# Optimization experiments

Measured on AMD Instinct MI355X. Metric: run time of the kernel, lower is better.

## Reference

```python
import jax, jax.numpy as jnp
import numpy as np

B, D_IN = 4096, 1024
E, K = 16, 2
EMB = 256
H1, H2 = 2048, 1024  # hidden_units, hidden_units // 2
O = 512              # num_classes


def setup_inputs() -> dict:
    key = jax.random.key(0)
    ks = jax.random.split(key, 10)
    s = lambda *sh: 1.0 / np.sqrt(sh[-2] if len(sh) > 1 else 1.0)
    return {
        "x":   jax.random.normal(ks[0], (B, D_IN), jnp.float32),
        "Wr":  jax.random.normal(ks[1], (D_IN, EMB), jnp.float32) * (1.0 / np.sqrt(D_IN)),
        "br":  jnp.zeros((EMB,), jnp.float32),
        "emb": jax.random.normal(ks[2], (E, EMB), jnp.float32) * (1.0 / np.sqrt(EMB)),
        "W1":  jax.random.normal(ks[3], (E, D_IN, H1), jnp.float32) * (1.0 / np.sqrt(D_IN)),
        "b1":  jnp.zeros((E, H1), jnp.float32),
        "W2":  jax.random.normal(ks[4], (E, H1, H2), jnp.float32) * (1.0 / np.sqrt(H1)),
        "b2":  jnp.zeros((E, H2), jnp.float32),
        "W3":  jax.random.normal(ks[5], (E, H2, O), jnp.float32) * (1.0 / np.sqrt(H2)),
        "b3":  jnp.zeros((E, O), jnp.float32),
    }


def reference(x, Wr, br, emb, W1, b1, W2, b2, W3, b3):
    # Router query: [B, EMB]
    q = x @ Wr + br
    # Negative squared euclidean distance to expert embeddings -> scores [B, E]
    d2 = jnp.sum(jnp.square(q[:, None, :] - emb[None, :, :]), axis=-1)
    scores = -d2
    gating_probs = jax.nn.softmax(scores, axis=-1)  # [B, E]
    # Top-k selection + renormalized gates
    top_v, top_i = jax.lax.top_k(scores, K)          # [B, K]
    gates = jax.nn.softmax(top_v, axis=-1)           # [B, K]
    # All experts run on full batch (dense), batched over expert axis
    h1 = jax.nn.relu(jnp.einsum('bi,eih->beh', x, W1) + b1)   # [B, E, H1]
    h2 = jax.nn.relu(jnp.einsum('beh,ehm->bem', h1, W2) + b2)  # [B, E, H2]
    out = jnp.einsum('bem,emo->beo', h2, W3) + b3              # [B, E, O]
    # Gather top-k expert outputs per example and combine
    sel = jnp.take_along_axis(out, top_i[:, :, None], axis=1)  # [B, K, O]
    final = jnp.sum(sel * gates[:, :, None], axis=1)           # [B, O]
    return final, q, gating_probs
```

## Files before the change

kernel.cpp:

```cpp
#include <hip/hip_runtime.h>
#include <hip/hip_bf16.h>

using bf16 = __hip_bfloat16;
typedef __attribute__((ext_vector_type(8))) short bf16x8;
typedef __attribute__((ext_vector_type(8))) unsigned short u16x8;
typedef __attribute__((ext_vector_type(4))) float f32x4;

constexpr int BATCH = 4096;
constexpr int D_IN  = 1024;
constexpr int NEXP  = 16;
constexpr int EMB   = 256;
constexpr int H1    = 2048;
constexpr int H2    = 1024;
constexpr int OUTD  = 512;
constexpr int SLOTS = BATCH * 2;
constexpr int SLOTS_PAD = SLOTS + 128;
constexpr int MAX_TILES = SLOTS / 128 + NEXP;

constexpr size_t WS_XB     = 0;
constexpr size_t WS_H1     = WS_XB     + (size_t)BATCH * D_IN * 2;
constexpr size_t WS_H2     = WS_H1     + (size_t)SLOTS_PAD * H1 * 2;
constexpr size_t WS_OSL    = WS_H2     + (size_t)SLOTS_PAD * H2 * 2;
constexpr size_t WS_TOPI   = WS_OSL    + (size_t)SLOTS_PAD * OUTD * 4;
constexpr size_t WS_GATES  = WS_TOPI   + (size_t)SLOTS * 4;
constexpr size_t WS_SLOTOF = WS_GATES  + (size_t)SLOTS * 4;
constexpr size_t WS_TOKL   = WS_SLOTOF + (size_t)SLOTS * 4;
constexpr size_t WS_CNT    = WS_TOKL   + (size_t)SLOTS_PAD * 4;
constexpr size_t WS_TMAP   = WS_CNT    + 64 * 4;
constexpr size_t WS_WT     = ((WS_TMAP + (size_t)MAX_TILES * 8) + 255) & ~(size_t)255;

__device__ __forceinline__ unsigned short f2bf(float f) {
    bf16 h = __float2bfloat16(f);
    return __builtin_bit_cast(unsigned short, h);
}

__device__ __forceinline__ void gload16(const unsigned short* g, unsigned short* l) {
    __builtin_amdgcn_global_load_lds(
        (const __attribute__((address_space(1))) unsigned int*)g,
        (__attribute__((address_space(3))) unsigned int*)l, 16, 0, 0);
}

__global__ __launch_bounds__(256) void k_cvt_x(const float* __restrict__ x,
                                               unsigned short* __restrict__ xb) {
    int i = blockIdx.x * 256 + threadIdx.x;
    float4 v = reinterpret_cast<const float4*>(x)[i];
    ushort4 o;
    o.x = f2bf(v.x); o.y = f2bf(v.y); o.z = f2bf(v.z); o.w = f2bf(v.w);
    reinterpret_cast<ushort4*>(xb)[i] = o;
}

__global__ __launch_bounds__(256) void k_wtrans(const float* __restrict__ W,
                                                unsigned short* __restrict__ Wt,
                                                int KD, int ND) {
    __shared__ float Tf[64][65];
    int e = blockIdx.z;
    int n0 = blockIdx.x * 64, k0 = blockIdx.y * 64;
    const float* Wb = W + ((size_t)e * KD + k0) * ND + n0;
    int t  = threadIdx.x;
    int kr = t >> 4, c4 = (t & 15) * 4;
#pragma unroll
    for (int i = 0; i < 4; i++) {
        float4 v = *reinterpret_cast<const float4*>(Wb + (size_t)(kr + i * 16) * ND + c4);
        Tf[kr + i * 16][c4 + 0] = v.x; Tf[kr + i * 16][c4 + 1] = v.y;
        Tf[kr + i * 16][c4 + 2] = v.z; Tf[kr + i * 16][c4 + 3] = v.w;
    }
    __syncthreads();
    unsigned short* Wtb = Wt + ((size_t)e * ND + n0) * KD + k0;
#pragma unroll
    for (int i = 0; i < 2; i++) {
        int idx = t + i * 256;
        int n = idx >> 3, ck = (idx & 7) * 8;
        u16x8 o;
#pragma unroll
        for (int j = 0; j < 8; j++) o[j] = f2bf(Tf[ck + j][n]);
        *reinterpret_cast<u16x8*>(Wtb + (size_t)n * KD + ck) = o;
    }
}

__global__ __launch_bounds__(256) void k_router_gemm(const float* __restrict__ x,
                                                     const float* __restrict__ Wr,
                                                     const float* __restrict__ br,
                                                     float* __restrict__ qout) {
    __shared__ float As[64][17];
    __shared__ float Bs[16][68];
    int mb = blockIdx.x * 64, nb = blockIdx.y * 64;
    int t  = threadIdx.x;
    int tx = t & 15, ty = t >> 4;
    float acc[4][4] = {};
    int arow = t >> 2, ak = (t & 3) * 4;
    int bkr = t >> 4, bnc = (t & 15) * 4;
    for (int kt = 0; kt < D_IN; kt += 16) {
        float4 av = *reinterpret_cast<const float4*>(&x[(size_t)(mb + arow) * D_IN + kt + ak]);
        float4 bv = *reinterpret_cast<const float4*>(&Wr[(size_t)(kt + bkr) * EMB + nb + bnc]);
        As[arow][ak + 0] = av.x; As[arow][ak + 1] = av.y;
        As[arow][ak + 2] = av.z; As[arow][ak + 3] = av.w;
        Bs[bkr][bnc + 0] = bv.x; Bs[bkr][bnc + 1] = bv.y;
        Bs[bkr][bnc + 2] = bv.z; Bs[bkr][bnc + 3] = bv.w;
        __syncthreads();
#pragma unroll
        for (int k = 0; k < 16; k++) {
            float a[4], bb[4];
#pragma unroll
            for (int i = 0; i < 4; i++) a[i] = As[ty * 4 + i][k];
#pragma unroll
            for (int j = 0; j < 4; j++) bb[j] = Bs[k][tx * 4 + j];
#pragma unroll
            for (int i = 0; i < 4; i++)
#pragma unroll
                for (int j = 0; j < 4; j++) acc[i][j] = fmaf(a[i], bb[j], acc[i][j]);
        }
        __syncthreads();
    }
#pragma unroll
    for (int i = 0; i < 4; i++) {
        int row = mb + ty * 4 + i;
        float4 o;
        o.x = acc[i][0] + br[nb + tx * 4 + 0];
        o.y = acc[i][1] + br[nb + tx * 4 + 1];
        o.z = acc[i][2] + br[nb + tx * 4 + 2];
        o.w = acc[i][3] + br[nb + tx * 4 + 3];
        *reinterpret_cast<float4*>(&qout[(size_t)row * EMB + nb + tx * 4]) = o;
    }
}

__global__ __launch_bounds__(256) void k_router_topk(const float* __restrict__ q,
                                                     const float* __restrict__ emb,
                                                     float* __restrict__ gp,
                                                     int* __restrict__ topi,
                                                     float* __restrict__ gates) {
    int b    = blockIdx.x * 4 + (threadIdx.x >> 6);
    int lane = threadIdx.x & 63;
    int e    = lane & 15;
    int seg  = (lane >> 4) * 64;
    const float* qr = q + (size_t)b * EMB + seg;
    const float* er = emb + (size_t)e * EMB + seg;
    float d2 = 0.f;
#pragma unroll 8
    for (int i = 0; i < 64; i++) { float d = qr[i] - er[i]; d2 = fmaf(d, d, d2); }
    d2 += __shfl_xor(d2, 16);
    d2 += __shfl_xor(d2, 32);
    float s = -d2;
    float m = s;
#pragma unroll
    for (int o = 1; o < 16; o <<= 1) m = fmaxf(m, __shfl_xor(m, o));
    float ex  = __expf(s - m);
    float sum = ex;
#pragma unroll
    for (int o = 1; o < 16; o <<= 1) sum += __shfl_xor(sum, o);
    if (lane < 16) gp[(size_t)b * NEXP + lane] = ex / sum;
    float v1 = s; int i1 = e;
#pragma unroll
    for (int o = 1; o < 16; o <<= 1) {
        float ov = __shfl_xor(v1, o); int oi = __shfl_xor(i1, o);
        if (ov > v1 || (ov == v1 && oi < i1)) { v1 = ov; i1 = oi; }
    }
    float s2 = (e == i1) ? -1e30f : s;
    float v2 = s2; int i2 = e;
#pragma unroll
    for (int o = 1; o < 16; o <<= 1) {
        float ov = __shfl_xor(v2, o); int oi = __shfl_xor(i2, o);
        if (ov > v2 || (ov == v2 && oi < i2)) { v2 = ov; i2 = oi; }
    }
    if (lane == 0) {
        topi[b * 2] = i1; topi[b * 2 + 1] = i2;
        float tv  = __expf(v2 - v1);
        float inv = 1.f / (1.f + tv);
        gates[b * 2] = inv; gates[b * 2 + 1] = tv * inv;
    }
}

__global__ void k_zero(int* counts) { if (threadIdx.x < NEXP) counts[threadIdx.x] = 0; }

__global__ __launch_bounds__(256) void k_count(const int* __restrict__ topi, int* __restrict__ counts) {
    int i = blockIdx.x * 256 + threadIdx.x;
    atomicAdd(&counts[topi[i]], 1);
}

__global__ void k_scan(const int* __restrict__ counts, int* __restrict__ offsets,
                       int* __restrict__ cursors, int2* __restrict__ tilemap) {
    if (threadIdx.x != 0) return;
    int off = 0, nt = 0;
    for (int e = 0; e < NEXP; e++) {
        offsets[e] = off; cursors[e] = off;
        int c = counts[e];
        int ntile = (c + 127) >> 7;
        for (int i = 0; i < ntile; i++) { tilemap[nt] = make_int2(e, i); nt++; }
        off += c;
    }
    for (; nt < MAX_TILES; nt++) tilemap[nt] = make_int2(-1, 0);
}

__global__ __launch_bounds__(256) void k_scatter(const int* __restrict__ topi, int* __restrict__ cursors,
                                                 int* __restrict__ toklist, int* __restrict__ slotof) {
    int i = blockIdx.x * 256 + threadIdx.x;
    int e = topi[i];
    int s = atomicAdd(&cursors[e], 1);
    toklist[s] = i >> 1;
    slotof[i]  = s;
}

template <int KD, int ND, int MODE>
__global__ __launch_bounds__(256) void k_expert_gemm(
    const unsigned short* __restrict__ Xin, const unsigned short* __restrict__ Wt,
    const float* __restrict__ bg, unsigned short* __restrict__ Hout,
    float* __restrict__ Oout, const int* __restrict__ counts,
    const int* __restrict__ offsets, const int* __restrict__ toklist,
    const int2* __restrict__ tilemap) {
    int2 tm = tilemap[blockIdx.y];
    int e = tm.x;
    if (e < 0) return;
    int mt  = tm.y;
    int n_e = counts[e];
    if (mt * 128 >= n_e) return;
    int off = offsets[e];
    int n0  = blockIdx.x * 128;

    __shared__ __align__(16) unsigned short As[128 * 64];
    __shared__ __align__(16) unsigned short Bs[128 * 64];

    int t    = threadIdx.x;
    int lane = t & 63;
    int w    = t >> 6;
    int wr   = (w >> 1) * 64;
    int wc   = (w & 1) * 64;

    int srow = lane >> 3;
    int swz  = (lane & 7) ^ srow;
    const unsigned short* asrc[4];
    const unsigned short* bsrc[4];
#pragma unroll
    for (int i = 0; i < 4; i++) {
        int r = i * 32 + w * 8 + srow;
        int g = mt * 128 + r;
        size_t arow;
        if (MODE == 0) {
            int gg = (g < n_e) ? g : (n_e - 1);
            arow = (size_t)toklist[off + gg];
        } else {
            arow = (size_t)(off + g);
        }
        asrc[i] = Xin + arow * KD + swz * 8;
        bsrc[i] = Wt + ((size_t)e * ND + n0 + r) * KD + swz * 8;
    }

    f32x4 acc[4][4];
#pragma unroll
    for (int mi = 0; mi < 4; mi++)
#pragma unroll
        for (int ni = 0; ni < 4; ni++) acc[mi][ni] = {0.f, 0.f, 0.f, 0.f};

    int lr  = lane & 15;
    int lkc = lane >> 4;

    for (int kt = 0; kt < KD; kt += 64) {
#pragma unroll
        for (int i = 0; i < 4; i++) {
            gload16(asrc[i] + kt, (unsigned short*)((char*)As + (i * 32 + w * 8) * 128) + lane * 8);
            gload16(bsrc[i] + kt, (unsigned short*)((char*)Bs + (i * 32 + w * 8) * 128) + lane * 8);
        }
        __syncthreads();
#pragma unroll
        for (int ks = 0; ks < 2; ks++) {
            bf16x8 a[4], b[4];
#pragma unroll
            for (int mi = 0; mi < 4; mi++) {
                int row = wr + mi * 16 + lr;
                int c   = (lkc + ks * 4) ^ (row & 7);
                a[mi] = *reinterpret_cast<const bf16x8*>((char*)As + row * 128 + c * 16);
            }
#pragma unroll
            for (int ni = 0; ni < 4; ni++) {
                int row = wc + ni * 16 + lr;
                int c   = (lkc + ks * 4) ^ (row & 7);
                b[ni] = *reinterpret_cast<const bf16x8*>((char*)Bs + row * 128 + c * 16);
            }
#pragma unroll
            for (int mi = 0; mi < 4; mi++)
#pragma unroll
                for (int ni = 0; ni < 4; ni++)
                    acc[mi][ni] = __builtin_amdgcn_mfma_f32_16x16x32_bf16(a[mi], b[ni], acc[mi][ni], 0, 0, 0);
        }
        __syncthreads();
    }

    int rowbase = (lane >> 4) * 4;
#pragma unroll
    for (int ni = 0; ni < 4; ni++) {
        int col = n0 + wc + ni * 16 + lr;
        float bv = bg[(size_t)e * ND + col];
#pragma unroll
        for (int mi = 0; mi < 4; mi++) {
#pragma unroll
            for (int qi = 0; qi < 4; qi++) {
                int g = mt * 128 + wr + mi * 16 + rowbase + qi;
                if (g < n_e) {
                    float v = acc[mi][ni][qi] + bv;
                    if (MODE == 2) {
                        Oout[(size_t)(off + g) * ND + col] = v;
                    } else {
                        v = fmaxf(v, 0.f);
                        Hout[(size_t)(off + g) * ND + col] = f2bf(v);
                    }
                }
            }
        }
    }
}

__global__ __launch_bounds__(128) void k_combine(const float* __restrict__ osl,
                                                 const float* __restrict__ gates,
                                                 const int* __restrict__ slotof,
                                                 float* __restrict__ outf) {
    int b = blockIdx.x;
    int j = threadIdx.x;
    int s0 = slotof[b * 2], s1 = slotof[b * 2 + 1];
    float g0 = gates[b * 2], g1 = gates[b * 2 + 1];
    float4 o0 = reinterpret_cast<const float4*>(osl + (size_t)s0 * OUTD)[j];
    float4 o1 = reinterpret_cast<const float4*>(osl + (size_t)s1 * OUTD)[j];
    float4 r;
    r.x = g0 * o0.x + g1 * o1.x;
    r.y = g0 * o0.y + g1 * o1.y;
    r.z = g0 * o0.z + g1 * o1.z;
    r.w = g0 * o0.w + g1 * o1.w;
    reinterpret_cast<float4*>(outf + (size_t)b * OUTD)[j] = r;
}

extern "C" void kernel_launch(void* const* d_in, const int* in_sizes, int n_in,
                              void* d_out, int out_size, void* d_ws, size_t ws_size,
                              hipStream_t stream) {
    const float* x   = (const float*)d_in[0];
    const float* Wr  = (const float*)d_in[1];
    const float* br  = (const float*)d_in[2];
    const float* emb = (const float*)d_in[3];
    const float* W1  = (const float*)d_in[4];
    const float* b1  = (const float*)d_in[5];
    const float* W2  = (const float*)d_in[6];
    const float* b2  = (const float*)d_in[7];
    const float* W3  = (const float*)d_in[8];
    const float* b3  = (const float*)d_in[9];

    float* out_final = (float*)d_out;
    float* out_q     = out_final + (size_t)BATCH * OUTD;
    float* out_gp    = out_q + (size_t)BATCH * EMB;

    char* ws = (char*)d_ws;
    unsigned short* xb  = (unsigned short*)(ws + WS_XB);
    unsigned short* h1  = (unsigned short*)(ws + WS_H1);
    unsigned short* h2  = (unsigned short*)(ws + WS_H2);
    float* osl    = (float*)(ws + WS_OSL);
    int*   topi   = (int*)(ws + WS_TOPI);
    float* gates  = (float*)(ws + WS_GATES);
    int*   slotof = (int*)(ws + WS_SLOTOF);
    int*   toklist= (int*)(ws + WS_TOKL);
    int*   counts = (int*)(ws + WS_CNT);
    int*   offsets= counts + 16;
    int*   cursors= counts + 32;
    int2*  tilemap= (int2*)(ws + WS_TMAP);
    unsigned short* wt = (unsigned short*)(ws + WS_WT);

    k_cvt_x<<<BATCH * D_IN / 4 / 256, 256, 0, stream>>>(x, xb);
    k_router_gemm<<<dim3(BATCH / 64, EMB / 64), 256, 0, stream>>>(x, Wr, br, out_q);
    k_router_topk<<<BATCH / 4, 256, 0, stream>>>(out_q, emb, out_gp, topi, gates);
    k_zero<<<1, 64, 0, stream>>>(counts);
    k_count<<<SLOTS / 256, 256, 0, stream>>>(topi, counts);
    k_scan<<<1, 64, 0, stream>>>(counts, offsets, cursors, tilemap);
    k_scatter<<<SLOTS / 256, 256, 0, stream>>>(topi, cursors, toklist, slotof);

    k_wtrans<<<dim3(H1 / 64, D_IN / 64, NEXP), 256, 0, stream>>>(W1, wt, D_IN, H1);
    k_expert_gemm<D_IN, H1, 0><<<dim3(H1 / 128, MAX_TILES), 256, 0, stream>>>(
        xb, wt, b1, h1, nullptr, counts, offsets, toklist, tilemap);

    k_wtrans<<<dim3(H2 / 64, H1 / 64, NEXP), 256, 0, stream>>>(W2, wt, H1, H2);
    k_expert_gemm<H1, H2, 1><<<dim3(H2 / 128, MAX_TILES), 256, 0, stream>>>(
        h1, wt, b2, h2, nullptr, counts, offsets, toklist, tilemap);

    k_wtrans<<<dim3(OUTD / 64, H2 / 64, NEXP), 256, 0, stream>>>(W3, wt, H2, OUTD);
    k_expert_gemm<H2, OUTD, 2><<<dim3(OUTD / 128, MAX_TILES), 256, 0, stream>>>(
        h2, wt, b3, nullptr, osl, counts, offsets, toklist, tilemap);

    k_combine<<<BATCH, 128, 0, stream>>>(osl, gates, slotof, out_final);
}
```

Before: 430.4 us.

## Double-buffer expert GEMM LDS tiles and bin expert tiles per XCD

The expert GEMM kernel now double-buffers its A/B shared-memory tiles, issuing the next K-slice's global loads before computing on the current one, which removes one barrier per iteration and hides load latency. The tile scheduler bins expert tiles into 8 groups, one per XCD, and remaps block ids so that blocks on the same XCD share expert weights in L2. Launch bounds now request 2 blocks per CU. In exchange, LDS use doubles to 64KB per block, which may limit occupancy, and the binning assumes round-robin dispatch of blocks across XCDs. It also caps each bin at MAX_TILES/8 tiles, so an unbalanced expert distribution could drop tiles.

After: 415.6 us. -3.4%, faster.

```diff
diff --git a/kernel.cpp b/kernel.cpp
--- a/kernel.cpp
+++ b/kernel.cpp
@@ -16,6 +16,7 @@
 constexpr int SLOTS = BATCH * 2;
 constexpr int SLOTS_PAD = SLOTS + 128;
 constexpr int MAX_TILES = SLOTS / 128 + NEXP;
+constexpr int BIN_CAP   = MAX_TILES / 8;
 
 constexpr size_t WS_XB     = 0;
 constexpr size_t WS_H1     = WS_XB     + (size_t)BATCH * D_IN * 2;
@@ -179,15 +180,29 @@
 __global__ void k_scan(const int* __restrict__ counts, int* __restrict__ offsets,
                        int* __restrict__ cursors, int2* __restrict__ tilemap) {
     if (threadIdx.x != 0) return;
-    int off = 0, nt = 0;
+    int off = 0;
+    int nt_e[NEXP];
     for (int e = 0; e < NEXP; e++) {
         offsets[e] = off; cursors[e] = off;
-        int c = counts[e];
-        int ntile = (c + 127) >> 7;
-        for (int i = 0; i < ntile; i++) { tilemap[nt] = make_int2(e, i); nt++; }
-        off += c;
-    }
-    for (; nt < MAX_TILES; nt++) tilemap[nt] = make_int2(-1, 0);
+        nt_e[e] = (counts[e] + 127) >> 7;
+        off += counts[e];
+    }
+    for (int i = 0; i < MAX_TILES; i++) tilemap[i] = make_int2(-1, 0);
+    int binload[8] = {0, 0, 0, 0, 0, 0, 0, 0};
+    for (int e = 0; e < NEXP; e++) {
+        int rem = nt_e[e], ti = 0;
+        while (rem > 0) {
+            int b = 0;
+            for (int q = 1; q < 8; q++)
+                if (binload[q] < binload[b]) b = q;
+            int space = BIN_CAP - binload[b];
+            if (space <= 0) break;
+            int take = (rem < space) ? rem : space;
+            for (int i = 0; i < take; i++)
+                tilemap[b * BIN_CAP + binload[b] + i] = make_int2(e, ti + i);
+            binload[b] += take; ti += take; rem -= take;
+        }
+    }
 }
 
 __global__ __launch_bounds__(256) void k_scatter(const int* __restrict__ topi, int* __restrict__ cursors,
@@ -200,23 +215,29 @@
 }
 
 template <int KD, int ND, int MODE>
-__global__ __launch_bounds__(256) void k_expert_gemm(
+__global__ __launch_bounds__(256, 2) void k_expert_gemm(
     const unsigned short* __restrict__ Xin, const unsigned short* __restrict__ Wt,
     const float* __restrict__ bg, unsigned short* __restrict__ Hout,
     float* __restrict__ Oout, const int* __restrict__ counts,
     const int* __restrict__ offsets, const int* __restrict__ toklist,
     const int2* __restrict__ tilemap) {
-    int2 tm = tilemap[blockIdx.y];
+    int id   = blockIdx.y * gridDim.x + blockIdx.x;
+    int cxcd = id & 7;
+    int jj   = id >> 3;
+    int y    = cxcd * BIN_CAP + jj % BIN_CAP;
+    int xnb  = jj / BIN_CAP;
+
+    int2 tm = tilemap[y];
     int e = tm.x;
     if (e < 0) return;
     int mt  = tm.y;
     int n_e = counts[e];
     if (mt * 128 >= n_e) return;
     int off = offsets[e];
-    int n0  = blockIdx.x * 128;
-
-    __shared__ __align__(16) unsigned short As[128 * 64];
-    __shared__ __align__(16) unsigned short Bs[128 * 64];
+    int n0  = xnb * 128;
+
+    __shared__ __align__(16) unsigned short As[2][128 * 64];
+    __shared__ __align__(16) unsigned short Bs[2][128 * 64];
 
     int t    = threadIdx.x;
     int lane = t & 63;
@@ -243,6 +264,14 @@
         bsrc[i] = Wt + ((size_t)e * ND + n0 + r) * KD + swz * 8;
     }
 
+    auto STAGE = [&](int buf, int kt) {
+#pragma unroll
+        for (int i = 0; i < 4; i++) {
+            gload16(asrc[i] + kt, &As[buf][(i * 32 + w * 8) * 64] + lane * 8);
+            gload16(bsrc[i] + kt, &Bs[buf][(i * 32 + w * 8) * 64] + lane * 8);
+        }
+    };
+
     f32x4 acc[4][4];
 #pragma unroll
     for (int mi = 0; mi < 4; mi++)
@@ -252,13 +281,15 @@
     int lr  = lane & 15;
     int lkc = lane >> 4;
 
-    for (int kt = 0; kt < KD; kt += 64) {
-#pragma unroll
-        for (int i = 0; i < 4; i++) {
-            gload16(asrc[i] + kt, (unsigned short*)((char*)As + (i * 32 + w * 8) * 128) + lane * 8);
-            gload16(bsrc[i] + kt, (unsigned short*)((char*)Bs + (i * 32 + w * 8) * 128) + lane * 8);
-        }
-        __syncthreads();
+    constexpr int T = KD / 64;
+    STAGE(0, 0);
+    __syncthreads();
+
+    for (int tt = 0; tt < T; tt++) {
+        int cur = tt & 1;
+        if (tt + 1 < T) STAGE(cur ^ 1, (tt + 1) * 64);
+        const char* Ab = (const char*)As[cur];
+        const char* Bb = (const char*)Bs[cur];
 #pragma unroll
         for (int ks = 0; ks < 2; ks++) {
             bf16x8 a[4], b[4];
@@ -266,13 +297,13 @@
             for (int mi = 0; mi < 4; mi++) {
                 int row = wr + mi * 16 + lr;
                 int c   = (lkc + ks * 4) ^ (row & 7);
-                a[mi] = *reinterpret_cast<const bf16x8*>((char*)As + row * 128 + c * 16);
+                a[mi] = *reinterpret_cast<const bf16x8*>(Ab + row * 128 + c * 16);
             }
 #pragma unroll
             for (int ni = 0; ni < 4; ni++) {
                 int row = wc + ni * 16 + lr;
                 int c   = (lkc + ks * 4) ^ (row & 7);
-                b[ni] = *reinterpret_cast<const bf16x8*>((char*)Bs + row * 128 + c * 16);
+                b[ni] = *reinterpret_cast<const bf16x8*>(Bb + row * 128 + c * 16);
             }
 #pragma unroll
             for (int mi = 0; mi < 4; mi++)
@@ -280,7 +311,7 @@
                 for (int ni = 0; ni < 4; ni++)
                     acc[mi][ni] = __builtin_amdgcn_mfma_f32_16x16x32_bf16(a[mi], b[ni], acc[mi][ni], 0, 0, 0);
         }
-        __syncthreads();
+        if (tt + 1 < T) __syncthreads();
     }
 
     int rowbase = (lane >> 4) * 4;
```
